# Performance work log

Hardware: AMD Instinct MI355X
Metric: run time of the kernel (lower is better)

## Reference

```python
import jax, jax.numpy as jnp
import numpy as np

B, S, E, H = 32, 4096, 256, 8
P, M = 256, 16  # positions per batch row, tokens per position (pileup depth)


def setup_inputs() -> dict:
    key = jax.random.key(0)
    k1, k2, k3, k4, k5, k6 = jax.random.split(key, 6)
    embeddings = jax.random.normal(k1, (B, S, E), jnp.float32)
    # each position 0..P-1 appears exactly M times per batch row, shuffled
    base = jnp.repeat(jnp.arange(P, dtype=jnp.int32), M)  # (S,)
    positions = jax.vmap(lambda k: jax.random.permutation(k, base))(jax.random.split(k2, B))
    scale = 1.0 / np.sqrt(E)
    Wq = jax.random.normal(k3, (E, E), jnp.float32) * scale
    Wk = jax.random.normal(k4, (E, E), jnp.float32) * scale
    Wv = jax.random.normal(k5, (E, E), jnp.float32) * scale
    W0 = jax.random.normal(k6, (E, E), jnp.float32) * scale
    return {"embeddings": embeddings, "Wq": Wq, "Wk": Wk, "Wv": Wv, "W0": W0,
            "positions": positions, "num_positions": P, "group_size": M, "num_heads": H}


def _intra_group_rank(positions):
    # rank[b,i] = number of earlier tokens j<i in row b with the same position
    Bb, Ss = positions.shape
    idx = jnp.arange(Ss)
    order = jnp.argsort(positions, axis=1)  # stable sort preserves original order within a group
    sp = jnp.take_along_axis(positions, order, axis=1)
    new_group = jnp.concatenate([jnp.ones((Bb, 1), bool), sp[:, 1:] != sp[:, :-1]], axis=1)
    group_start = jax.lax.cummax(jnp.where(new_group, idx[None, :], 0), axis=1)
    rank_sorted = idx[None, :] - group_start
    rank = jnp.zeros_like(positions).at[jnp.arange(Bb)[:, None], order].set(rank_sorted.astype(positions.dtype))
    return rank


def reference(embeddings, Wq, Wk, Wv, W0, positions, num_positions, group_size, num_heads):
    Bb, Ss, Ee = embeddings.shape
    Pp, Mm, Hh = num_positions, group_size, num_heads
    dh = Ee // Hh
    G = Bb * Pp

    valid = positions >= 0
    rank = _intra_group_rank(positions)                       # (B,S) slot within group
    gid = jnp.arange(Bb, dtype=positions.dtype)[:, None] * Pp + jnp.clip(positions, 0)  # (B,S)
    gid_scat = jnp.where(valid, gid, G)                        # out-of-bounds -> dropped

    # gather: ragged regroup into (G, M, E), zero-padded like the torch version
    grouped = jnp.zeros((G, Mm, Ee), embeddings.dtype).at[gid_scat, rank].set(embeddings, mode='drop')

    # multi-head self-attention within each group (no mask, matching the original)
    q = (grouped @ Wq).reshape(G, Mm, Hh, dh)
    k = (grouped @ Wk).reshape(G, Mm, Hh, dh)
    v = (grouped @ Wv).reshape(G, Mm, Hh, dh)
    scores = jnp.einsum('gmhd,gnhd->ghmn', q, k) / np.sqrt(dh).astype(embeddings.dtype)
    attn = jax.nn.softmax(scores, axis=-1)
    ctx = jnp.einsum('ghmn,gnhd->gmhd', attn, v).reshape(G, Mm, Ee)
    att_out = ctx @ W0                                         # (G, M, E)

    # scatter back; invalid (-1) slots stay zero, as in the torch loop
    out = jnp.where(valid[:, :, None], att_out[gid, rank], 0.0)
    return out
```

## Files before the change

kernel.cpp:

```cpp
#include <hip/hip_runtime.h>
#include <stdint.h>

#define B_    32
#define S_    4096
#define E_    256
#define P_    256
#define M_    16
#define G_    (B_*P_)
#define NSLOT (G_*M_)
#define GPW   8
#define ROWS  128
#define NWG   (G_/GPW)

typedef float fv4 __attribute__((ext_vector_type(4)));
typedef int   iv4 __attribute__((ext_vector_type(4)));
typedef int   iv2 __attribute__((ext_vector_type(2)));
typedef __bf16 bv8 __attribute__((ext_vector_type(8)));
typedef short  sv4 __attribute__((ext_vector_type(4)));

__device__ __forceinline__ uint32_t bf16rne(float f) {
  uint32_t u = __builtin_bit_cast(uint32_t, f);
  u += 0x7fffu + ((u >> 16) & 1u);
  return u >> 16;
}
__device__ __forceinline__ uint32_t pk2(uint32_t lo, uint32_t hi) {
  return (lo & 0xffffu) | (hi << 16);
}
__device__ __forceinline__ void mfma32(fv4& d, iv4 a, iv4 b) {
  d = __builtin_amdgcn_mfma_f32_16x16x32_bf16(
        __builtin_bit_cast(bv8, a), __builtin_bit_cast(bv8, b), d, 0, 0, 0);
}
__device__ __forceinline__ void mfma16(fv4& d, iv2 a, iv2 b) {
  d = __builtin_amdgcn_mfma_f32_16x16x16bf16_1k(
        __builtin_bit_cast(sv4, a), __builtin_bit_cast(sv4, b), d, 0, 0, 0);
}
__device__ __forceinline__ void gload_lds16(const void* g, void* l) {
  __builtin_amdgcn_global_load_lds(
      (const __attribute__((address_space(1))) uint32_t*)g,
      (__attribute__((address_space(3))) uint32_t*)l, 16, 0, 0);
}

#define SWZ(off, row) ((off) ^ (((row) & 7) << 4))
#define LQKV(row, cb) ( ((row) >> 1) * 128 + \
    (((((row) & 1) << 6) + (cb)) ^ ((((row) >> 1) & 7) << 4)) )

#define BAR()   { asm volatile("" ::: "memory"); __builtin_amdgcn_s_barrier(); \
                  asm volatile("" ::: "memory"); }
#define VMWAIT2 asm volatile("s_waitcnt vmcnt(2)" ::: "memory")
#define VMWAIT0 asm volatile("s_waitcnt vmcnt(0)" ::: "memory")
#define LGKM0   asm volatile("s_waitcnt lgkmcnt(0)" ::: "memory")

__global__ void k_init(int* cnt, int* s2t) {
  int i = blockIdx.x * 256 + threadIdx.x;
  if (i < G_) cnt[i] = 0;
  if (i < NSLOT) s2t[i] = -1;
}

__global__ void k_trans(const float* __restrict__ Wq, const float* __restrict__ Wk,
                        const float* __restrict__ Wv, const float* __restrict__ W0,
                        uint16_t* __restrict__ WT) {
  int o = blockIdx.x * 256 + threadIdx.x;
  int wsel = blockIdx.y;
  const float* W = (wsel == 0) ? Wq : (wsel == 1) ? Wk : (wsel == 2) ? Wv : W0;
  int n = o >> 8, k = o & 255;
  WT[(size_t)wsel * 65536 + o] = (uint16_t)bf16rne(W[k * 256 + n]);
}

__global__ void k_rank(const int* __restrict__ pos, int* cnt, int* s2t) {
  int i = blockIdx.x * 256 + threadIdx.x;
  if (i >= B_ * S_) return;
  int p = pos[i];
  if (p < 0 || p >= P_) return;
  int b = i >> 12;
  int g = (b << 8) + p;
  int r = atomicAdd(&cnt[g], 1);
  if (r < M_) s2t[g * M_ + r] = i;
}

__device__ __forceinline__ void stage_qkv(const uint16_t* Wt, int c0, char* buf,
                                          int w, int l) {
  #pragma unroll
  for (int it = 0; it < 2; ++it) {
    int q = it * 8 + w;
    int n = q * 2 + (l >> 5);
    int seg = l & 31;
    gload_lds16(reinterpret_cast<const char*>(Wt) + (size_t)(c0 + n) * 512 + SWZ(seg * 16, n),
                buf + q * 1024);
  }
}
__device__ __forceinline__ void stage_w0(const uint16_t* W0T, int c0, char* buf,
                                         int w, int l) {
  #pragma unroll
  for (int it = 0; it < 2; ++it) {
    int q = it * 8 + w;
    int pair = q * 8 + (l >> 3);
    int jp = ((l & 7) * 16) ^ ((pair & 7) << 4);
    int n = 2 * pair + (jp >> 6);
    gload_lds16(reinterpret_cast<const char*>(W0T) + (size_t)n * 512 + c0 * 2 + (jp & 63),
                buf + q * 1024);
  }
}

__global__ __launch_bounds__(512, 2) void k_main(
    const float* __restrict__ emb, const int* __restrict__ s2t,
    const uint16_t* __restrict__ WT, float* __restrict__ out) {
  extern __shared__ char smem[];
  char* bufA = smem;
  char* bufB = smem + 16384;
  char* Qb = smem + 32768;
  char* Kb = smem + 40960;
  char* Vb = smem + 49152;
  char* Cb = smem + 57344;

  const uint16_t* WqT = WT;
  const uint16_t* WkT = WT + 65536;
  const uint16_t* WvT = WT + 131072;
  const uint16_t* W0T = WT + 196608;

  const int tid = threadIdx.x;
  const int l = tid & 63;
  const int w = tid >> 6;
  const int lane15 = l & 15;
  const int lq = l >> 4;
  const int mq2 = w >> 1;
  const int nh = w & 1;
  const int slot0 = blockIdx.x * ROWS;

  #pragma unroll 2
  for (int rl = 0; rl < 16; ++rl) {
    int row = w * 16 + rl;
    int t = s2t[slot0 + row];
    uint32_t u0 = 0, u1 = 0;
    if (t >= 0) {
      const float4 v = *reinterpret_cast<const float4*>(emb + (size_t)t * E_ + (l << 2));
      u0 = pk2(bf16rne(v.x), bf16rne(v.y));
      u1 = pk2(bf16rne(v.z), bf16rne(v.w));
    }
    iv2 val; val[0] = (int)u0; val[1] = (int)u1;
    *reinterpret_cast<iv2*>(smem + row * 512 + SWZ(l * 8, row)) = val;
  }
  __syncthreads();

  iv4 xf[8];
  const int arow = w * 16 + lane15;
  #pragma unroll
  for (int ks = 0; ks < 8; ++ks)
    xf[ks] = *reinterpret_cast<const iv4*>(smem + arow * 512 + SWZ(ks * 64 + lq * 16, arow));
  __syncthreads();

  fv4 outacc[2][8];
  #pragma unroll
  for (int a = 0; a < 2; ++a)
    #pragma unroll
    for (int b = 0; b < 8; ++b) outacc[a][b] = fv4{0.f, 0.f, 0.f, 0.f};

  stage_qkv(WqT, 0, bufA, w, l);
  stage_qkv(WkT, 0, bufB, w, l);

  for (int hc = 0; hc < 8; ++hc) {
    const int c0 = hc * 32;

    #define COMPUTE_QKV(buf, dst)                                            \
    {                                                                        \
      fv4 a0 = fv4{0.f,0.f,0.f,0.f}, a1 = fv4{0.f,0.f,0.f,0.f};              \
      const int n0 = lane15, n1 = lane15 + 16;                               \
      _Pragma("unroll")                                                      \
      for (int ks = 0; ks < 8; ++ks) {                                       \
        iv4 b0 = *reinterpret_cast<const iv4*>((buf) + n0 * 512 + SWZ(ks * 64 + lq * 16, n0)); \
        iv4 b1 = *reinterpret_cast<const iv4*>((buf) + n1 * 512 + SWZ(ks * 64 + lq * 16, n1)); \
        mfma32(a0, xf[ks], b0);                                              \
        mfma32(a1, xf[ks], b1);                                              \
      }                                                                      \
      _Pragma("unroll")                                                      \
      for (int r = 0; r < 4; ++r) {                                          \
        int row = w * 16 + lq * 4 + r;                                       \
        *reinterpret_cast<uint16_t*>((dst) + LQKV(row, lane15 * 2)) =        \
            (uint16_t)bf16rne(a0[r]);                                        \
        *reinterpret_cast<uint16_t*>((dst) + LQKV(row, (lane15 + 16) * 2)) = \
            (uint16_t)bf16rne(a1[r]);                                        \
      }                                                                      \
    }

    VMWAIT2; BAR();
    COMPUTE_QKV(bufA, Qb);
    LGKM0; BAR();
    stage_qkv(WvT, c0, bufA, w, l);

    VMWAIT2; BAR();
    COMPUTE_QKV(bufB, Kb);
    LGKM0; BAR();
    stage_w0(W0T, c0, bufB, w, l);

    VMWAIT2; BAR();
    COMPUTE_QKV(bufA, Vb);
    LGKM0; BAR();
    if (hc < 7) stage_qkv(WqT, c0 + 32, bufA, w, l);

    {
      const int frow = w * 16 + lane15;
      iv4 kf = *reinterpret_cast<const iv4*>(Kb + LQKV(frow, lq * 16));
      iv4 qf = *reinterpret_cast<const iv4*>(Qb + LQKV(frow, lq * 16));
      fv4 s = fv4{0.f, 0.f, 0.f, 0.f};
      mfma32(s, kf, qf);
      float mx = fmaxf(fmaxf(s[0], s[1]), fmaxf(s[2], s[3]));
      mx = fmaxf(mx, __shfl_xor(mx, 16));
      mx = fmaxf(mx, __shfl_xor(mx, 32));
      const float Cc = 0.25503373f;
      float e0 = exp2f((s[0] - mx) * Cc), e1 = exp2f((s[1] - mx) * Cc);
      float e2 = exp2f((s[2] - mx) * Cc), e3 = exp2f((s[3] - mx) * Cc);
      float sum = e0 + e1 + e2 + e3;
      sum += __shfl_xor(sum, 16);
      sum += __shfl_xor(sum, 32);
      float inv = 1.0f / sum;
      iv2 pa; pa[0] = (int)pk2(bf16rne(e0 * inv), bf16rne(e1 * inv));
              pa[1] = (int)pk2(bf16rne(e2 * inv), bf16rne(e3 * inv));
      const int r0 = w * 16 + lq * 4;
      #pragma unroll
      for (int dvt = 0; dvt < 2; ++dvt) {
        int cb = (dvt * 16 + lane15) * 2;
        uint32_t v0 = *reinterpret_cast<const uint16_t*>(Vb + LQKV(r0 + 0, cb));
        uint32_t v1 = *reinterpret_cast<const uint16_t*>(Vb + LQKV(r0 + 1, cb));
        uint32_t v2 = *reinterpret_cast<const uint16_t*>(Vb + LQKV(r0 + 2, cb));
        uint32_t v3 = *reinterpret_cast<const uint16_t*>(Vb + LQKV(r0 + 3, cb));
        iv2 bv; bv[0] = (int)pk2(v0, v1); bv[1] = (int)pk2(v2, v3);
        fv4 cacc = fv4{0.f, 0.f, 0.f, 0.f};
        mfma16(cacc, pa, bv);
        #pragma unroll
        for (int r = 0; r < 4; ++r)
          *reinterpret_cast<uint16_t*>(Cb + LQKV(r0 + r, cb)) =
              (uint16_t)bf16rne(cacc[r]);
      }
    }

    if (hc < 7) { VMWAIT2; } else { VMWAIT0; }
    LGKM0; BAR();
    #pragma unroll
    for (int mt = 0; mt < 2; ++mt) {
      int ar = mq2 * 32 + mt * 16 + lane15;
      iv4 af = *reinterpret_cast<const iv4*>(Cb + LQKV(ar, lq * 16));
      #pragma unroll
      for (int nt = 0; nt < 8; ++nt) {
        int n = nh * 128 + nt * 16 + lane15;
        iv4 bfg = *reinterpret_cast<const iv4*>(
            bufB + (n >> 1) * 128 + ((((n & 1) << 6) + lq * 16) ^ (((n >> 1) & 7) << 4)));
        mfma32(outacc[mt][nt], af, bfg);
      }
    }
    BAR();
    if (hc < 7) stage_qkv(WkT, c0 + 32, bufB, w, l);
    #undef COMPUTE_QKV
  }

  #pragma unroll
  for (int mt = 0; mt < 2; ++mt) {
    int rb = mq2 * 32 + mt * 16 + lq * 4;
    int t0 = s2t[slot0 + rb + 0];
    int t1 = s2t[slot0 + rb + 1];
    int t2 = s2t[slot0 + rb + 2];
    int t3 = s2t[slot0 + rb + 3];
    #pragma unroll
    for (int nt = 0; nt < 8; ++nt) {
      int col = nh * 128 + nt * 16 + lane15;
      if (t0 >= 0) out[(size_t)t0 * E_ + col] = outacc[mt][nt][0];
      if (t1 >= 0) out[(size_t)t1 * E_ + col] = outacc[mt][nt][1];
      if (t2 >= 0) out[(size_t)t2 * E_ + col] = outacc[mt][nt][2];
      if (t3 >= 0) out[(size_t)t3 * E_ + col] = outacc[mt][nt][3];
    }
  }
}

extern "C" void kernel_launch(void* const* d_in, const int* in_sizes, int n_in,
                              void* d_out, int out_size, void* d_ws, size_t ws_size,
                              hipStream_t stream) {
  (void)in_sizes; (void)n_in; (void)out_size; (void)ws_size;
  const float* emb = (const float*)d_in[0];
  const float* Wq  = (const float*)d_in[1];
  const float* Wk  = (const float*)d_in[2];
  const float* Wv  = (const float*)d_in[3];
  const float* W0  = (const float*)d_in[4];
  const int*   pos = (const int*)d_in[5];
  float* out = (float*)d_out;

  int* cnt = (int*)d_ws;
  int* s2t = (int*)((char*)d_ws + 32768);
  uint16_t* WT = (uint16_t*)((char*)d_ws + 32768 + 524288);

  (void)hipFuncSetAttribute(reinterpret_cast<const void*>(k_main),
                            hipFuncAttributeMaxDynamicSharedMemorySize, 65536);

  k_init <<<512, 256, 0, stream>>>(cnt, s2t);
  k_trans<<<dim3(256, 4), 256, 0, stream>>>(Wq, Wk, Wv, W0, WT);
  k_rank <<<512, 256, 0, stream>>>(pos, cnt, s2t);
  k_main <<<NWG, 512, 65536, stream>>>(emb, s2t, WT, out);
}
```

Baseline: 178.8 us.

## Double workgroup to 1024 threads, splitting head columns across wave pairs

Workgroups now have 16 waves instead of 8. Each wave pair splits the 32 head columns (Q/K/V projections and the PV product) and the output columns for one 16-row block, and each wave handles one staging load instead of two. The aim is more waves in flight per workgroup to hide latency, with fewer accumulator registers per thread. The trade-off is a launch bound of one 1024-thread block per CU, where before two 512-thread blocks could share it. Each wave also redundantly recomputes the QK softmax for its row block.

```diff
diff --git a/kernel.cpp b/kernel.cpp
--- a/kernel.cpp
+++ b/kernel.cpp
@@ -46,7 +46,7 @@
 
 #define BAR()   { asm volatile("" ::: "memory"); __builtin_amdgcn_s_barrier(); \
                   asm volatile("" ::: "memory"); }
-#define VMWAIT2 asm volatile("s_waitcnt vmcnt(2)" ::: "memory")
+#define VMWAIT1 asm volatile("s_waitcnt vmcnt(1)" ::: "memory")
 #define VMWAIT0 asm volatile("s_waitcnt vmcnt(0)" ::: "memory")
 #define LGKM0   asm volatile("s_waitcnt lgkmcnt(0)" ::: "memory")
 
@@ -79,29 +79,21 @@
 
 __device__ __forceinline__ void stage_qkv(const uint16_t* Wt, int c0, char* buf,
                                           int w, int l) {
-  #pragma unroll
-  for (int it = 0; it < 2; ++it) {
-    int q = it * 8 + w;
-    int n = q * 2 + (l >> 5);
-    int seg = l & 31;
-    gload_lds16(reinterpret_cast<const char*>(Wt) + (size_t)(c0 + n) * 512 + SWZ(seg * 16, n),
-                buf + q * 1024);
-  }
+  int n = w * 2 + (l >> 5);
+  int seg = l & 31;
+  gload_lds16(reinterpret_cast<const char*>(Wt) + (size_t)(c0 + n) * 512 + SWZ(seg * 16, n),
+              buf + w * 1024);
 }
 __device__ __forceinline__ void stage_w0(const uint16_t* W0T, int c0, char* buf,
                                          int w, int l) {
-  #pragma unroll
-  for (int it = 0; it < 2; ++it) {
-    int q = it * 8 + w;
-    int pair = q * 8 + (l >> 3);
-    int jp = ((l & 7) * 16) ^ ((pair & 7) << 4);
-    int n = 2 * pair + (jp >> 6);
-    gload_lds16(reinterpret_cast<const char*>(W0T) + (size_t)n * 512 + c0 * 2 + (jp & 63),
-                buf + q * 1024);
-  }
-}
-
-__global__ __launch_bounds__(512, 2) void k_main(
+  int pair = w * 8 + (l >> 3);
+  int jp = ((l & 7) * 16) ^ ((pair & 7) << 4);
+  int n = 2 * pair + (jp >> 6);
+  gload_lds16(reinterpret_cast<const char*>(W0T) + (size_t)n * 512 + c0 * 2 + (jp & 63),
+              buf + w * 1024);
+}
+
+__global__ __launch_bounds__(1024, 1) void k_main(
     const float* __restrict__ emb, const int* __restrict__ s2t,
     const uint16_t* __restrict__ WT, float* __restrict__ out) {
   extern __shared__ char smem[];
@@ -122,13 +114,13 @@
   const int w = tid >> 6;
   const int lane15 = l & 15;
   const int lq = l >> 4;
-  const int mq2 = w >> 1;
-  const int nh = w & 1;
+  const int rb = w >> 1;
+  const int ch = w & 1;
   const int slot0 = blockIdx.x * ROWS;
 
   #pragma unroll 2
-  for (int rl = 0; rl < 16; ++rl) {
-    int row = w * 16 + rl;
+  for (int rl = 0; rl < 8; ++rl) {
+    int row = w * 8 + rl;
     int t = s2t[slot0 + row];
     uint32_t u0 = 0, u1 = 0;
     if (t >= 0) {
@@ -142,17 +134,15 @@
   __syncthreads();
 
   iv4 xf[8];
-  const int arow = w * 16 + lane15;
+  const int arow = rb * 16 + lane15;
   #pragma unroll
   for (int ks = 0; ks < 8; ++ks)
     xf[ks] = *reinterpret_cast<const iv4*>(smem + arow * 512 + SWZ(ks * 64 + lq * 16, arow));
   __syncthreads();
 
-  fv4 outacc[2][8];
+  fv4 outacc[8];
   #pragma unroll
-  for (int a = 0; a < 2; ++a)
-    #pragma unroll
-    for (int b = 0; b < 8; ++b) outacc[a][b] = fv4{0.f, 0.f, 0.f, 0.f};
+  for (int i = 0; i < 8; ++i) outacc[i] = fv4{0.f, 0.f, 0.f, 0.f};
 
   stage_qkv(WqT, 0, bufA, w, l);
   stage_qkv(WkT, 0, bufB, w, l);
@@ -162,42 +152,38 @@
 
     #define COMPUTE_QKV(buf, dst)                                            \
     {                                                                        \
-      fv4 a0 = fv4{0.f,0.f,0.f,0.f}, a1 = fv4{0.f,0.f,0.f,0.f};              \
-      const int n0 = lane15, n1 = lane15 + 16;                               \
+      fv4 a0 = fv4{0.f,0.f,0.f,0.f};                                         \
+      const int n0 = ch * 16 + lane15;                                       \
       _Pragma("unroll")                                                      \
       for (int ks = 0; ks < 8; ++ks) {                                       \
         iv4 b0 = *reinterpret_cast<const iv4*>((buf) + n0 * 512 + SWZ(ks * 64 + lq * 16, n0)); \
-        iv4 b1 = *reinterpret_cast<const iv4*>((buf) + n1 * 512 + SWZ(ks * 64 + lq * 16, n1)); \
         mfma32(a0, xf[ks], b0);                                              \
-        mfma32(a1, xf[ks], b1);                                              \
       }                                                                      \
       _Pragma("unroll")                                                      \
       for (int r = 0; r < 4; ++r) {                                          \
-        int row = w * 16 + lq * 4 + r;                                       \
-        *reinterpret_cast<uint16_t*>((dst) + LQKV(row, lane15 * 2)) =        \
+        int row = rb * 16 + lq * 4 + r;                                      \
+        *reinterpret_cast<uint16_t*>((dst) + LQKV(row, n0 * 2)) =            \
             (uint16_t)bf16rne(a0[r]);                                        \
-        *reinterpret_cast<uint16_t*>((dst) + LQKV(row, (lane15 + 16) * 2)) = \
-            (uint16_t)bf16rne(a1[r]);                                        \
       }                                                                      \
     }
 
-    VMWAIT2; BAR();
+    VMWAIT1; BAR();
     COMPUTE_QKV(bufA, Qb);
     LGKM0; BAR();
     stage_qkv(WvT, c0, bufA, w, l);
 
-    VMWAIT2; BAR();
+    VMWAIT1; BAR();
     COMPUTE_QKV(bufB, Kb);
     LGKM0; BAR();
     stage_w0(W0T, c0, bufB, w, l);
 
-    VMWAIT2; BAR();
+    VMWAIT1; BAR();
     COMPUTE_QKV(bufA, Vb);
     LGKM0; BAR();
     if (hc < 7) stage_qkv(WqT, c0 + 32, bufA, w, l);
 
     {
-      const int frow = w * 16 + lane15;
+      const int frow = rb * 16 + lane15;
       iv4 kf = *reinterpret_cast<const iv4*>(Kb + LQKV(frow, lq * 16));
       iv4 qf = *reinterpret_cast<const iv4*>(Qb + LQKV(frow, lq * 16));
       fv4 s = fv4{0.f, 0.f, 0.f, 0.f};
@@ -214,36 +200,32 @@
       float inv = 1.0f / sum;
       iv2 pa; pa[0] = (int)pk2(bf16rne(e0 * inv), bf16rne(e1 * inv));
               pa[1] = (int)pk2(bf16rne(e2 * inv), bf16rne(e3 * inv));
-      const int r0 = w * 16 + lq * 4;
+      const int r0 = rb * 16 + lq * 4;
+      const int cb = (ch * 16 + lane15) * 2;
+      uint32_t v0 = *reinterpret_cast<const uint16_t*>(Vb + LQKV(r0 + 0, cb));
+      uint32_t v1 = *reinterpret_cast<const uint16_t*>(Vb + LQKV(r0 + 1, cb));
+      uint32_t v2 = *reinterpret_cast<const uint16_t*>(Vb + LQKV(r0 + 2, cb));
+      uint32_t v3 = *reinterpret_cast<const uint16_t*>(Vb + LQKV(r0 + 3, cb));
+      iv2 bv; bv[0] = (int)pk2(v0, v1); bv[1] = (int)pk2(v2, v3);
+      fv4 cacc = fv4{0.f, 0.f, 0.f, 0.f};
+      mfma16(cacc, pa, bv);
       #pragma unroll
-      for (int dvt = 0; dvt < 2; ++dvt) {
-        int cb = (dvt * 16 + lane15) * 2;
-        uint32_t v0 = *reinterpret_cast<const uint16_t*>(Vb + LQKV(r0 + 0, cb));
-        uint32_t v1 = *reinterpret_cast<const uint16_t*>(Vb + LQKV(r0 + 1, cb));
-        uint32_t v2 = *reinterpret_cast<const uint16_t*>(Vb + LQKV(r0 + 2, cb));
-        uint32_t v3 = *reinterpret_cast<const uint16_t*>(Vb + LQKV(r0 + 3, cb));
-        iv2 bv; bv[0] = (int)pk2(v0, v1); bv[1] = (int)pk2(v2, v3);
-        fv4 cacc = fv4{0.f, 0.f, 0.f, 0.f};
-        mfma16(cacc, pa, bv);
-        #pragma unroll
-        for (int r = 0; r < 4; ++r)
-          *reinterpret_cast<uint16_t*>(Cb + LQKV(r0 + r, cb)) =
-              (uint16_t)bf16rne(cacc[r]);
-      }
-    }
-
-    if (hc < 7) { VMWAIT2; } else { VMWAIT0; }
-    LGKM0; BAR();
-    #pragma unroll
-    for (int mt = 0; mt < 2; ++mt) {
-      int ar = mq2 * 32 + mt * 16 + lane15;
+      for (int r = 0; r < 4; ++r)
+        *reinterpret_cast<uint16_t*>(Cb + LQKV(r0 + r, cb)) =
+            (uint16_t)bf16rne(cacc[r]);
+    }
+
+    if (hc < 7) { VMWAIT1; } else { VMWAIT0; }
+    LGKM0; BAR();
+    {
+      int ar = rb * 16 + lane15;
       iv4 af = *reinterpret_cast<const iv4*>(Cb + LQKV(ar, lq * 16));
       #pragma unroll
       for (int nt = 0; nt < 8; ++nt) {
-        int n = nh * 128 + nt * 16 + lane15;
+        int n = ch * 128 + nt * 16 + lane15;
         iv4 bfg = *reinterpret_cast<const iv4*>(
             bufB + (n >> 1) * 128 + ((((n & 1) << 6) + lq * 16) ^ (((n >> 1) & 7) << 4)));
-        mfma32(outacc[mt][nt], af, bfg);
+        mfma32(outacc[nt], af, bfg);
       }
     }
     BAR();
@@ -252,19 +234,13 @@
   }
 
   #pragma unroll
-  for (int mt = 0; mt < 2; ++mt) {
-    int rb = mq2 * 32 + mt * 16 + lq * 4;
-    int t0 = s2t[slot0 + rb + 0];
-    int t1 = s2t[slot0 + rb + 1];
-    int t2 = s2t[slot0 + rb + 2];
-    int t3 = s2t[slot0 + rb + 3];
+  for (int r = 0; r < 4; ++r) {
+    int t = s2t[slot0 + rb * 16 + lq * 4 + r];
+    if (t < 0) continue;
     #pragma unroll
     for (int nt = 0; nt < 8; ++nt) {
-      int col = nh * 128 + nt * 16 + lane15;
-      if (t0 >= 0) out[(size_t)t0 * E_ + col] = outacc[mt][nt][0];
-      if (t1 >= 0) out[(size_t)t1 * E_ + col] = outacc[mt][nt][1];
-      if (t2 >= 0) out[(size_t)t2 * E_ + col] = outacc[mt][nt][2];
-      if (t3 >= 0) out[(size_t)t3 * E_ + col] = outacc[mt][nt][3];
+      int col = ch * 128 + nt * 16 + lane15;
+      out[(size_t)t * E_ + col] = outacc[nt][r];
     }
   }
 }
@@ -291,5 +267,5 @@
   k_init <<<512, 256, 0, stream>>>(cnt, s2t);
   k_trans<<<dim3(256, 4), 256, 0, stream>>>(Wq, Wk, Wv, W0, WT);
   k_rank <<<512, 256, 0, stream>>>(pos, cnt, s2t);
-  k_main <<<NWG, 512, 65536, stream>>>(emb, s2t, WT, out);
-}
+  k_main <<<NWG, 1024, 65536, stream>>>(emb, s2t, WT, out);
+}
```

Result: no change. 177.4 us (-0.8%).
